# Kernel tuning notes

Hardware: AMD Instinct MI355X
Metric: run time of the kernel (lower is better)

The kernel has to match this reference:

```python
import jax, jax.numpy as jnp
import numpy as np

GLOBAL = 3
BETA = 10
CR, CO, CS = 9, 2, 1
N_PCA = 45
PARENTS = [0, 1, 2, 0, 4, 5, 0, 7, 8, 0, 10, 11, 0, 13, 14]
JOINT_REORDER_MESH = {4: 743, 8: 333, 12: 443, 16: 555, 20: 678}


def rodrigues(r):
    # r: [..., 3] axis-angle -> [..., 3, 3] rotation matrix
    theta = jnp.sqrt(jnp.sum(r * r, axis=-1, keepdims=True) + 1e-8)
    n = r / theta
    th = theta[..., None]
    c, s = jnp.cos(th), jnp.sin(th)
    nx, ny, nz = n[..., 0], n[..., 1], n[..., 2]
    z = jnp.zeros_like(nx)
    K = jnp.stack([z, -nz, ny, nz, z, -nx, -ny, nx, z], axis=-1).reshape(r.shape[:-1] + (3, 3))
    outer = n[..., :, None] * n[..., None, :]
    eye = jnp.eye(3, dtype=r.dtype)
    return c * eye + (1.0 - c) * outer + s * K


def setup_inputs() -> dict:
    key = jax.random.key(0)
    ks = jax.random.split(key, 12)
    B, T, D = 32, 128, 5376
    out_dim = N_PCA + GLOBAL + BETA + CR + CO + CS  # 70
    return {
        "x": jax.random.normal(ks[0], (B, T, D), dtype=jnp.float32),
        "W": jax.random.normal(ks[1], (out_dim, D), dtype=jnp.float32) * 0.01,
        "b": jax.random.normal(ks[2], (out_dim,), dtype=jnp.float32) * 0.01,
        "hand_ppal_comps": jax.random.normal(ks[3], (N_PCA, 45), dtype=jnp.float32) * 0.1,
        "mean_hand": jax.random.normal(ks[4], (45,), dtype=jnp.float32) * 0.1,
        "hand_template": jax.random.normal(ks[5], (778, 3), dtype=jnp.float32) * 0.05,
        "shapedirs": jax.random.normal(ks[6], (778, 3, 10), dtype=jnp.float32) * 0.01,
        "posedirs": jax.random.normal(ks[7], (778, 3, 135), dtype=jnp.float32) * 0.01,
        "J_reg": jax.random.uniform(ks[8], (16, 778), dtype=jnp.float32) / 778.0,
        "lbs_weights": jax.nn.softmax(jax.random.normal(ks[9], (778, 16), dtype=jnp.float32), axis=-1),
    }


def _forward(x, W, b, hand_ppal_comps, mean_hand, hand_template, shapedirs, posedirs, J_reg, lbs_weights):
    N, T, _ = x.shape
    params = x @ W.T + b  # [N,T,70]
    n_pca = hand_ppal_comps.shape[0]
    off = GLOBAL + n_pca
    theta = params[..., :off]
    beta = params[..., off:off + BETA]
    c_r = params[..., off + BETA:off + BETA + CR]
    c_o = params[..., off + BETA + CR:off + BETA + CR + CO]
    c_s = params[..., off + BETA + CR + CO:off + BETA + CR + CO + CS]

    # pose from PCA
    hand_posed = theta[..., GLOBAL:] @ hand_ppal_comps + mean_hand  # [N,T,45]
    hand_posed = jnp.concatenate([theta[..., :GLOBAL], hand_posed], axis=-1)  # [N,T,48]

    # shape blendshapes and joints
    hand_shaped = jnp.einsum('vck,btk->btvc', shapedirs, beta) + hand_template  # [N,T,778,3]
    J = jnp.einsum('jv,btvc->btjc', J_reg, hand_shaped)  # [N,T,16,3]

    # pose blendshapes (lrotmin: flattened Rodrigues matrices of the 15 finger joints)
    rod135 = rodrigues(hand_posed[..., GLOBAL:].reshape(N, T, 15, 3)).reshape(N, T, 135)
    curr_hand = hand_shaped + jnp.einsum('vck,btk->btvc', posedirs, rod135)

    # global rigid transformation (kinematic tree)
    rot16 = rodrigues(hand_posed.reshape(N, T, 16, 3))  # [N,T,16,3,3]
    row = jnp.broadcast_to(jnp.array([0.0, 0.0, 0.0, 1.0], dtype=x.dtype), (N, T, 1, 4))
    T0 = jnp.concatenate([jnp.concatenate([rot16[:, :, 0], J[:, :, 0, :, None]], axis=-1), row], axis=-2)  # [N,T,4,4]
    parents = np.array(PARENTS)
    rel = (J[:, :, 1:] - J[:, :, parents])[..., None]  # [N,T,15,3,1]
    op = jnp.concatenate([rot16[:, :, 1:], rel], axis=-1)  # [N,T,15,3,4]
    row15 = jnp.broadcast_to(jnp.array([0.0, 0.0, 0.0, 1.0], dtype=x.dtype), (N, T, 15, 1, 4))
    op = jnp.concatenate([op, row15], axis=-2)  # [N,T,15,4,4]
    res = [T0]
    for i in range(15):
        res.append(res[PARENTS[i]] @ op[:, :, i])
    results = jnp.stack(res, axis=2)  # [N,T,16,4,4]

    ext_J = jnp.concatenate([J, jnp.zeros((N, T, 16, 1), dtype=x.dtype)], axis=-1)
    corr = jnp.einsum('btjik,btjk->btji', results, ext_J)  # [N,T,16,4]
    A = results - jnp.concatenate([jnp.zeros((N, T, 16, 4, 3), dtype=x.dtype), corr[..., None]], axis=-1)
    J3d = results[..., :3, 3]  # [N,T,16,3]

    # linear blend skinning
    Tv = jnp.einsum('btjik,vj->btvik', A, lbs_weights)  # [N,T,778,4,4]
    curr_h = jnp.concatenate([curr_hand, jnp.ones((N, T, 778, 1), dtype=x.dtype)], axis=-1)
    mesh = jnp.einsum('btvij,btvj->btvi', Tv, curr_h)[..., :3]  # [N,T,778,3]

    jr = lambda i: J3d[:, :, i]
    mv = lambda v: mesh[:, :, v]
    J3d_re = jnp.stack([jr(0), jr(13), jr(14), jr(15), mv(743), jr(1), jr(2), jr(3), mv(333),
                        jr(4), jr(5), jr(6), mv(443), jr(10), jr(11), jr(12), mv(555),
                        jr(7), jr(8), jr(9), mv(678)], axis=2)  # [N,T,21,3]

    c_r3 = c_r.reshape(N, T, 3, 3)
    J2d = (J3d_re @ c_r3)[..., :2]
    J2d = c_s[:, :, None] * J2d + c_o[:, :, None]
    return (J2d, theta, beta)


def reference(x, W, b, hand_ppal_comps, mean_hand, hand_template, shapedirs, posedirs, J_reg, lbs_weights):
    return _forward(x, W, b, hand_ppal_comps, mean_hand, hand_template, shapedirs, posedirs, J_reg, lbs_weights)
```

## Files before the change

### kernel.cpp

```cpp
#include <hip/hip_runtime.h>
#include <hip/hip_bf16.h>

typedef short short8 __attribute__((ext_vector_type(8)));
typedef float float4_ __attribute__((ext_vector_type(4)));
typedef unsigned short ushort_t;

#define OUT_THETA 172032
#define OUT_BETA  368640
#define NROW 4096
#define KDIM 5376
#define NPAD 80
#define KS 24
#define NCHUNK 7

__device__ __constant__ int c_jslot[16] = {0,5,6,7,9,10,11,17,18,19,13,14,15,1,2,3};
__device__ __constant__ int c_vslot[5]  = {4,8,12,16,20};

__device__ inline short f2bf(float f) {
  union { float f; unsigned u; } v; v.f = f;
  unsigned r = v.u + 0x7fffu + ((v.u >> 16) & 1u);
  return (short)(r >> 16);
}

__device__ inline short8 cvt8(float4_ a, float4_ b) {
  short8 r;
  r[0]=f2bf(a[0]); r[1]=f2bf(a[1]); r[2]=f2bf(a[2]); r[3]=f2bf(a[3]);
  r[4]=f2bf(b[0]); r[5]=f2bf(b[1]); r[6]=f2bf(b[2]); r[7]=f2bf(b[3]);
  return r;
}

__global__ __launch_bounds__(256) void setup_kernel(
    const float* __restrict__ W, const float* __restrict__ shapedirs,
    const float* __restrict__ posedirs, const float* __restrict__ Jreg,
    const float* __restrict__ tmpl, const float* __restrict__ lbs,
    ushort_t* __restrict__ wfrag, float* __restrict__ jsd, float* __restrict__ jt,
    float* __restrict__ psel, float* __restrict__ ssel, float* __restrict__ tsel,
    float* __restrict__ wsel)
{
  int b = blockIdx.x, t = threadIdx.x;
  if (b < 210) {
    int idx = b*256 + t;
    int n = idx / 672, kg = idx % 672;
    short8 o;
    if (n < 70) {
      const float* wp = W + (size_t)n*KDIM + kg*8;
      float4_ w0 = *(const float4_*)wp;
      float4_ w1 = *(const float4_*)(wp+4);
      o = cvt8(w0, w1);
    } else {
      o = (short8){0,0,0,0,0,0,0,0};
    }
    *(short8*)(wfrag + ((size_t)kg*NPAD + n)*8) = o;
  } else if (b < 342) {
    int wv = (b-210)*4 + (t>>6);
    int l = t & 63;
    float p = 0.f;
    if (wv < 480) {
      int j = wv/30, r = wv%30, c = r/10, kk = r%10;
      for (int v = l; v < 778; v += 64) p += Jreg[j*778+v]*shapedirs[(v*3+c)*10+kk];
    } else {
      int o = wv-480; int j = o/3, c = o%3;
      for (int v = l; v < 778; v += 64) p += Jreg[j*778+v]*tmpl[v*3+c];
    }
    for (int off = 32; off > 0; off >>= 1) p += __shfl_down(p, off);
    if (l == 0) { if (wv < 480) jsd[wv] = p; else jt[wv-480] = p; }
  } else {
    const int vtx[5] = {743,333,443,555,678};
    for (int s = t; s < 2270; s += 256) {
      if (s < 2025) { int vi = s/405, r = s%405, c = r/135, kk = r%135;
        psel[s] = posedirs[((size_t)vtx[vi]*3 + c)*135 + kk]; }
      else if (s < 2175) { int u = s-2025; int vi = u/30, r = u%30, c = r/10, kk = r%10;
        ssel[u] = shapedirs[((size_t)vtx[vi]*3 + c)*10 + kk]; }
      else if (s < 2190) { int u = s-2175; int vi = u/3, c = u%3;
        tsel[u] = tmpl[vtx[vi]*3 + c]; }
      else if (s < 2270) { int u = s-2190; int vi = u/16, j = u%16;
        wsel[u] = lbs[vtx[vi]*16 + j]; }
    }
  }
}

__global__ __launch_bounds__(128) void gemm_params(
    const float* __restrict__ x, const ushort_t* __restrict__ wfrag,
    float* __restrict__ part)
{
  int gw = (blockIdx.x << 1) + (threadIdx.x >> 6);
  int l = threadIdx.x & 63;
  int rg = gw & 255;
  int kq = gw >> 8;
  int m0 = rg << 4;
  int k0 = kq * (NCHUNK*32);
  int q = l >> 4, lm = l & 15;

  const float* ap = x + (size_t)(m0 + lm)*KDIM + k0 + q*8;
  const ushort_t* bp = wfrag + ((size_t)((k0>>3) + q)*NPAD + lm)*8;

  float4_ acc0 = {0.f,0.f,0.f,0.f}, acc1 = acc0, acc2 = acc0, acc3 = acc0, acc4 = acc0;

  float4_ a0[4], a1[4];
  short8  bb[2][5];

  #pragma unroll
  for (int s = 0; s < 4; ++s) {
    a0[s] = *(const float4_*)(ap + s*32);
    a1[s] = *(const float4_*)(ap + s*32 + 4);
  }
  #pragma unroll
  for (int s = 0; s < 2; ++s) {
    #pragma unroll
    for (int n = 0; n < 5; ++n)
      bb[s][n] = *(const short8*)(bp + (size_t)s*(4*NPAD*8) + n*128);
  }

  #pragma unroll
  for (int c = 0; c < NCHUNK; ++c) {
    const int s = c & 3, sb = c & 1;
    short8 af = cvt8(a0[s], a1[s]);
    if (c + 4 < NCHUNK) {
      a0[s] = *(const float4_*)(ap + (c+4)*32);
      a1[s] = *(const float4_*)(ap + (c+4)*32 + 4);
    }
    acc0 = __builtin_amdgcn_mfma_f32_16x16x32_bf16(af, bb[sb][0], acc0, 0, 0, 0);
    acc1 = __builtin_amdgcn_mfma_f32_16x16x32_bf16(af, bb[sb][1], acc1, 0, 0, 0);
    acc2 = __builtin_amdgcn_mfma_f32_16x16x32_bf16(af, bb[sb][2], acc2, 0, 0, 0);
    acc3 = __builtin_amdgcn_mfma_f32_16x16x32_bf16(af, bb[sb][3], acc3, 0, 0, 0);
    acc4 = __builtin_amdgcn_mfma_f32_16x16x32_bf16(af, bb[sb][4], acc4, 0, 0, 0);
    if (c + 2 < NCHUNK) {
      #pragma unroll
      for (int n = 0; n < 5; ++n)
        bb[sb][n] = *(const short8*)(bp + (size_t)(c+2)*(4*NPAD*8) + n*128);
    }
  }

  float* op = part + ((size_t)kq*NROW + m0 + q*4)*NPAD + lm;
  #pragma unroll
  for (int r = 0; r < 4; ++r) {
    op[(size_t)r*NPAD +  0] = acc0[r];
    op[(size_t)r*NPAD + 16] = acc1[r];
    op[(size_t)r*NPAD + 32] = acc2[r];
    op[(size_t)r*NPAD + 48] = acc3[r];
    op[(size_t)r*NPAD + 64] = acc4[r];
  }
}

__global__ __launch_bounds__(64) void decode_kernel(
    const float* __restrict__ part, const float* __restrict__ bvec,
    const float* __restrict__ comps, const float* __restrict__ meanh,
    const float* __restrict__ jsd, const float* __restrict__ jt,
    const float* __restrict__ psel, const float* __restrict__ ssel,
    const float* __restrict__ tsel, const float* __restrict__ wsel,
    float* __restrict__ out)
{
  int row = blockIdx.x;
  int l = threadIdx.x;
  __shared__ float P[70];
  __shared__ float HP[48];
  __shared__ float R[16][9];
  __shared__ float Jl[48];
  __shared__ float RES[16][16];
  __shared__ float Al[16][16];
  __shared__ float CH[5][4];
  __shared__ float M3[21][3];

  {
    float v = bvec[l];
    #pragma unroll
    for (int k = 0; k < KS; ++k) v += part[((size_t)k*NROW + row)*NPAD + l];
    P[l] = v;
    if (l < 48) out[OUT_THETA + (size_t)row*48 + l] = v;
    else if (l < 58) out[OUT_BETA + (size_t)row*10 + (l-48)] = v;
    if (l < 6) {
      int c2 = l + 64;
      float w = bvec[c2];
      #pragma unroll
      for (int k = 0; k < KS; ++k) w += part[((size_t)k*NROW + row)*NPAD + c2];
      P[c2] = w;
    }
  }
  __syncthreads();

  if (l < 45) {
    float s = meanh[l];
    for (int k = 0; k < 45; ++k) s += P[3+k]*comps[k*45 + l];
    HP[3+l] = s;
  } else if (l < 48) HP[l-45] = P[l-45];
  __syncthreads();

  if (l < 16) {
    float rx = HP[3*l], ry = HP[3*l+1], rz = HP[3*l+2];
    float th = sqrtf(rx*rx + ry*ry + rz*rz + 1e-8f);
    float inv = 1.0f/th;
    float nx = rx*inv, ny = ry*inv, nz = rz*inv;
    float cth = cosf(th), sth = sinf(th), mc = 1.0f - cth;
    R[l][0] = cth + mc*nx*nx;     R[l][1] = mc*nx*ny - sth*nz;  R[l][2] = mc*nx*nz + sth*ny;
    R[l][3] = mc*ny*nx + sth*nz;  R[l][4] = cth + mc*ny*ny;     R[l][5] = mc*ny*nz - sth*nx;
    R[l][6] = mc*nz*nx - sth*ny;  R[l][7] = mc*nz*ny + sth*nx;  R[l][8] = cth + mc*nz*nz;
  }
  if (l < 48) {
    float s = jt[l];
    #pragma unroll
    for (int k = 0; k < 10; ++k) s += jsd[l*10+k]*P[48+k];
    Jl[l] = s;
  }
  __syncthreads();

  if (l < 16) {
    int r = l >> 2, c = l & 3;
    RES[0][l] = (r < 3) ? ((c < 3) ? R[0][3*r+c] : Jl[r]) : ((c == 3) ? 1.f : 0.f);
  }
  __syncthreads();
  constexpr int PARS[15] = {0,1,2,0,4,5,0,7,8,0,10,11,0,13,14};
  #pragma unroll
  for (int i = 0; i < 15; ++i) {
    const int p = PARS[i];
    if (l < 16) {
      int r = l >> 2, c = l & 3;
      float s = (c == 3) ? RES[p][4*r+3] : 0.f;
      #pragma unroll
      for (int k = 0; k < 3; ++k) {
        float opv = (c < 3) ? R[i+1][3*k+c] : (Jl[3*(i+1)+k] - Jl[3*p+k]);
        s += RES[p][4*r+k]*opv;
      }
      RES[i+1][l] = s;
    }
    __syncthreads();
  }

  {
    int j = l >> 2, r = l & 3;
    float corr = RES[j][4*r]*Jl[3*j] + RES[j][4*r+1]*Jl[3*j+1] + RES[j][4*r+2]*Jl[3*j+2];
    Al[j][4*r+0] = RES[j][4*r+0];
    Al[j][4*r+1] = RES[j][4*r+1];
    Al[j][4*r+2] = RES[j][4*r+2];
    Al[j][4*r+3] = RES[j][4*r+3] - corr;
  }
  if (l < 15) {
    int vi = l/3, ci = l%3;
    float s = tsel[l];
    #pragma unroll
    for (int k = 0; k < 10; ++k) s += ssel[l*10+k]*P[48+k];
    for (int j15 = 0; j15 < 15; ++j15) {
      #pragma unroll
      for (int e = 0; e < 9; ++e) s += psel[l*135 + j15*9 + e]*R[j15+1][e];
    }
    CH[vi][ci] = s;
  }
  __syncthreads();

  if (l < 48) {
    int j = l/3, c = l%3;
    M3[c_jslot[j]][c] = RES[j][4*c+3];
  } else if (l < 63) {
    int s0 = l - 48; int vi = s0/3, r = s0%3;
    float m = 0.f;
    #pragma unroll
    for (int j = 0; j < 16; ++j) {
      float tv = Al[j][4*r]*CH[vi][0] + Al[j][4*r+1]*CH[vi][1]
               + Al[j][4*r+2]*CH[vi][2] + Al[j][4*r+3];
      m += wsel[vi*16+j]*tv;
    }
    M3[c_vslot[vi]][r] = m;
  }
  __syncthreads();

  if (l < 42) {
    int k = l >> 1, d = l & 1;
    float s = M3[k][0]*P[58 + d] + M3[k][1]*P[58 + 3 + d] + M3[k][2]*P[58 + 6 + d];
    out[((size_t)row*21 + k)*2 + d] = P[69]*s + P[67+d];
  }
}

extern "C" void kernel_launch(void* const* d_in, const int* in_sizes, int n_in,
                              void* d_out, int out_size, void* d_ws, size_t ws_size,
                              hipStream_t stream) {
  const float* x         = (const float*)d_in[0];
  const float* W         = (const float*)d_in[1];
  const float* bvec      = (const float*)d_in[2];
  const float* comps     = (const float*)d_in[3];
  const float* meanh     = (const float*)d_in[4];
  const float* tmpl      = (const float*)d_in[5];
  const float* shapedirs = (const float*)d_in[6];
  const float* posedirs  = (const float*)d_in[7];
  const float* Jreg      = (const float*)d_in[8];
  const float* lbs       = (const float*)d_in[9];

  const size_t PART_ONE = (size_t)NROW*NPAD*4;

  char* ws = (char*)d_ws;
  float*    part  = (float*)ws;
  ushort_t* wfrag = (ushort_t*)(ws + (size_t)KS*PART_ONE);
  char*     tb    = ws + (size_t)KS*PART_ONE + 860160;
  float* jsd  = (float*)tb;
  float* jt   = (float*)(tb + 1920);
  float* psel = (float*)(tb + 1920 + 192);
  float* ssel = (float*)(tb + 1920 + 192 + 8100);
  float* tsel = (float*)(tb + 1920 + 192 + 8100 + 600);
  float* wsel = (float*)(tb + 1920 + 192 + 8100 + 600 + 60);
  float* out  = (float*)d_out;

  hipLaunchKernelGGL(setup_kernel, dim3(343), dim3(256), 0, stream,
                     W, shapedirs, posedirs, Jreg, tmpl, lbs,
                     wfrag, jsd, jt, psel, ssel, tsel, wsel);
  hipLaunchKernelGGL(gemm_params, dim3(3072), dim3(128), 0, stream,
                     x, wfrag, part);
  hipLaunchKernelGGL(decode_kernel, dim3(4096), dim3(64), 0, stream,
                     part, bvec, comps, meanh, jsd, jt, psel, ssel, tsel, wsel, out);
}
```

Before: 189.1 us.

## Stage bf16-converted x tiles in LDS and cut split-K count

The GEMM kernel now loads a 64-row by 384-column x tile per 256-thread block with coalesced reads, converts it to bf16 once and stores it in padded shared memory, then each wave reads its A fragments from LDS. Split-K drops from 24 to 14 slices with 12 MFMA chunks per wave, which shrinks the partial-sum buffer the decode kernel must reduce. The cost is a full-tile load before a barrier with no overlap of global loads and MFMA, about 49KB of LDS per block that limits occupancy, and fewer blocks in flight.

```diff
diff --git a/kernel.cpp b/kernel.cpp
--- a/kernel.cpp
+++ b/kernel.cpp
@@ -10,8 +10,9 @@
 #define NROW 4096
 #define KDIM 5376
 #define NPAD 80
-#define KS 24
-#define NCHUNK 7
+#define KS 14
+#define KCH 12
+#define LDS_STRIDE 392
 
 __device__ __constant__ int c_jslot[16] = {0,5,6,7,9,10,11,17,18,19,13,14,15,1,2,3};
 __device__ __constant__ int c_vslot[5]  = {4,8,12,16,20};
@@ -79,31 +80,44 @@
   }
 }
 
-__global__ __launch_bounds__(128) void gemm_params(
+__global__ __launch_bounds__(256) void gemm_params(
     const float* __restrict__ x, const ushort_t* __restrict__ wfrag,
     float* __restrict__ part)
 {
-  int gw = (blockIdx.x << 1) + (threadIdx.x >> 6);
-  int l = threadIdx.x & 63;
-  int rg = gw & 255;
-  int kq = gw >> 8;
-  int m0 = rg << 4;
-  int k0 = kq * (NCHUNK*32);
+  __shared__ ushort_t As[64*LDS_STRIDE];
+  int t = threadIdx.x;
+  int rb = blockIdx.x & 63;
+  int kq = blockIdx.x >> 6;
+  int m_base = rb << 6;
+  int k0 = kq * (KCH*32);
+
+  #pragma unroll
+  for (int h = 0; h < 2; ++h) {
+    float4_ u0[6], u1[6];
+    int dst[6];
+    #pragma unroll
+    for (int j = 0; j < 6; ++j) {
+      int flat = (h*6 + j)*256 + t;
+      int row = flat / 48, g = flat - row*48;
+      const float* p = x + (size_t)(m_base + row)*KDIM + k0 + g*8;
+      u0[j] = *(const float4_*)p;
+      u1[j] = *(const float4_*)(p + 4);
+      dst[j] = row*LDS_STRIDE + g*8;
+    }
+    #pragma unroll
+    for (int j = 0; j < 6; ++j)
+      *(short8*)&As[dst[j]] = cvt8(u0[j], u1[j]);
+  }
+  __syncthreads();
+
+  int l = t & 63, w = t >> 6;
   int q = l >> 4, lm = l & 15;
-
-  const float* ap = x + (size_t)(m0 + lm)*KDIM + k0 + q*8;
   const ushort_t* bp = wfrag + ((size_t)((k0>>3) + q)*NPAD + lm)*8;
+  const ushort_t* arow = &As[(w*16 + lm)*LDS_STRIDE + q*8];
 
   float4_ acc0 = {0.f,0.f,0.f,0.f}, acc1 = acc0, acc2 = acc0, acc3 = acc0, acc4 = acc0;
 
-  float4_ a0[4], a1[4];
-  short8  bb[2][5];
-
-  #pragma unroll
-  for (int s = 0; s < 4; ++s) {
-    a0[s] = *(const float4_*)(ap + s*32);
-    a1[s] = *(const float4_*)(ap + s*32 + 4);
-  }
+  short8 bb[2][5];
   #pragma unroll
   for (int s = 0; s < 2; ++s) {
     #pragma unroll
@@ -112,25 +126,22 @@
   }
 
   #pragma unroll
-  for (int c = 0; c < NCHUNK; ++c) {
-    const int s = c & 3, sb = c & 1;
-    short8 af = cvt8(a0[s], a1[s]);
-    if (c + 4 < NCHUNK) {
-      a0[s] = *(const float4_*)(ap + (c+4)*32);
-      a1[s] = *(const float4_*)(ap + (c+4)*32 + 4);
-    }
+  for (int c = 0; c < KCH; ++c) {
+    const int sb = c & 1;
+    short8 af = *(const short8*)(arow + c*32);
     acc0 = __builtin_amdgcn_mfma_f32_16x16x32_bf16(af, bb[sb][0], acc0, 0, 0, 0);
     acc1 = __builtin_amdgcn_mfma_f32_16x16x32_bf16(af, bb[sb][1], acc1, 0, 0, 0);
     acc2 = __builtin_amdgcn_mfma_f32_16x16x32_bf16(af, bb[sb][2], acc2, 0, 0, 0);
     acc3 = __builtin_amdgcn_mfma_f32_16x16x32_bf16(af, bb[sb][3], acc3, 0, 0, 0);
     acc4 = __builtin_amdgcn_mfma_f32_16x16x32_bf16(af, bb[sb][4], acc4, 0, 0, 0);
-    if (c + 2 < NCHUNK) {
+    if (c + 2 < KCH) {
       #pragma unroll
       for (int n = 0; n < 5; ++n)
         bb[sb][n] = *(const short8*)(bp + (size_t)(c+2)*(4*NPAD*8) + n*128);
     }
   }
 
+  int m0 = m_base + w*16;
   float* op = part + ((size_t)kq*NROW + m0 + q*4)*NPAD + lm;
   #pragma unroll
   for (int r = 0; r < 4; ++r) {
@@ -300,7 +311,7 @@
   hipLaunchKernelGGL(setup_kernel, dim3(343), dim3(256), 0, stream,
                      W, shapedirs, posedirs, Jreg, tmpl, lbs,
                      wfrag, jsd, jt, psel, ssel, tsel, wsel);
-  hipLaunchKernelGGL(gemm_params, dim3(3072), dim3(128), 0, stream,
+  hipLaunchKernelGGL(gemm_params, dim3(64*KS), dim3(256), 0, stream,
                      x, wfrag, part);
   hipLaunchKernelGGL(decode_kernel, dim3(4096), dim3(64), 0, stream,
                      part, bvec, comps, meanh, jsd, jt, psel, ssel, tsel, wsel, out);
```

After: 184.0 us. -2.7%, faster.
